# Optimization experiments

Measured on AMD Instinct MI355X. Metric: run time of the kernel, lower is better.

Reference implementation:

```python
import jax, jax.numpy as jnp
import numpy as np
from jax import lax

B, N = 8, 8192
H, W = 512, 512
C = 192          # backbone feature channels (Swin-L stage 1)
HF, WF = 128, 128  # H/4, W/4
STATE = 256
VLR = 3
STRIDE = 4.0
DOWN = 4.0
EPS = 1e-8


def bilinear_sample(feat, poly, h, w):
    """F.grid_sample(align_corners=True, bilinear) equivalent.
    feat: (B,C,h,w), poly: (B,N,2) pixel coords -> (B,C,N)."""
    gx = poly[..., 0] / (w / 2.0) - 1.0
    gy = poly[..., 1] / (h / 2.0) - 1.0
    x = (gx + 1.0) * 0.5 * (w - 1)   # align_corners=True unnormalize
    y = (gy + 1.0) * 0.5 * (h - 1)
    x0 = jnp.floor(x); y0 = jnp.floor(y)
    fx = x - x0; fy = y - y0
    x0i = jnp.clip(x0, 0, w - 1).astype(jnp.int32)
    x1i = jnp.clip(x0 + 1, 0, w - 1).astype(jnp.int32)
    y0i = jnp.clip(y0, 0, h - 1).astype(jnp.int32)
    y1i = jnp.clip(y0 + 1, 0, h - 1).astype(jnp.int32)
    b = jnp.arange(feat.shape[0])[:, None]
    f00 = feat[b, :, y0i, x0i]  # (B,N,C)
    f01 = feat[b, :, y0i, x1i]
    f10 = feat[b, :, y1i, x0i]
    f11 = feat[b, :, y1i, x1i]
    w00 = ((1 - fy) * (1 - fx))[..., None]
    w01 = ((1 - fy) * fx)[..., None]
    w10 = (fy * (1 - fx))[..., None]
    w11 = (fy * fx)[..., None]
    out = f00 * w00 + f01 * w01 + f10 * w10 + f11 * w11  # (B,N,C)
    return jnp.transpose(out, (0, 2, 1))  # (B,C,N)


def mlp3(x, W1, b1, W2, b2, W3, b3):
    """per-point MLP (1x1 conv stack). x: (B,Cin,N) -> (B,Cout,N)."""
    h1 = jax.nn.relu(jnp.einsum('oc,bcn->bon', W1, x) + b1[None, :, None])
    h2 = jax.nn.relu(jnp.einsum('oc,bcn->bon', W2, h1) + b2[None, :, None])
    return jnp.einsum('oc,bcn->bon', W3, h2) + b3[None, :, None]


def can_poly(poly, mask):
    # canonical poly: subtract per-polygon masked min of valid points
    big = jnp.float32(1e9)
    masked = jnp.where(mask[..., None] > 0, poly, big)
    mins = jnp.min(masked, axis=1, keepdims=True)  # (B,1,2)
    return (poly - mins) * mask[..., None]


def polygon_angles(poly, mask):
    prev = jnp.roll(poly, 1, axis=1)
    nxt = jnp.roll(poly, -1, axis=1)
    v1 = prev - poly
    v2 = nxt - poly
    dot = jnp.sum(v1 * v2, axis=-1)
    nrm = jnp.linalg.norm(v1, axis=-1) * jnp.linalg.norm(v2, axis=-1)
    cosang = jnp.clip(dot / (nrm + EPS), -1.0, 1.0)
    return jnp.arccos(cosang) * mask  # (B,N)


def setup_inputs() -> dict:
    key = jax.random.key(0)
    ks = jax.random.split(key, 20)
    DIN_OFF = C + 2   # 194
    DIN_CLS = C + 3   # 195
    inp = {
        'image': jax.random.normal(ks[0], (B, 3, H, W), jnp.float32),
        'pred_points': jax.random.uniform(ks[1], (B, N, 2), jnp.float32) * (WF - 1),
        'valid_mask': jnp.ones((B, N), jnp.float32),
        'bw': jax.random.normal(ks[2], (C, 3, 4, 4), jnp.float32) * 0.05,
        'bb': jnp.zeros((C,), jnp.float32),
        'off_W1': jax.random.normal(ks[3], (VLR, STATE, DIN_OFF), jnp.float32) * 0.02,
        'off_b1': jnp.zeros((VLR, STATE), jnp.float32),
        'off_W2': jax.random.normal(ks[4], (VLR, STATE, STATE), jnp.float32) * 0.02,
        'off_b2': jnp.zeros((VLR, STATE), jnp.float32),
        'off_W3': jax.random.normal(ks[5], (VLR, 2, STATE), jnp.float32) * 0.02,
        'off_b3': jnp.zeros((VLR, 2), jnp.float32),
        'cls_W1': jax.random.normal(ks[6], (STATE, DIN_CLS), jnp.float32) * 0.02,
        'cls_b1': jnp.zeros((STATE,), jnp.float32),
        'cls_W2': jax.random.normal(ks[7], (STATE, STATE), jnp.float32) * 0.02,
        'cls_b2': jnp.zeros((STATE,), jnp.float32),
        'cls_W3': jax.random.normal(ks[8], (1, STATE), jnp.float32) * 0.02,
        'cls_b3': jnp.zeros((1,), jnp.float32),
    }
    return inp


def reference(image, pred_points, valid_mask, bw, bb,
              off_W1, off_b1, off_W2, off_b2, off_W3, off_b3,
              cls_W1, cls_b1, cls_W2, cls_b2, cls_W3, cls_b3):
    # frozen backbone stand-in (torch.no_grad on swin_l): stride-4 patch-embed conv
    feat = lax.conv_general_dilated(
        image, bw, window_strides=(4, 4), padding='VALID',
        dimension_numbers=('NCHW', 'OIHW', 'NCHW')) + bb[None, :, None, None]
    feat = lax.stop_gradient(feat)  # (B,C,HF,WF)

    py = pred_points
    for i in range(VLR):
        c_py = can_poly(py, valid_mask)
        g = bilinear_sample(feat, py, HF, WF) * valid_mask[:, None, :]   # (B,C,N)
        x = jnp.concatenate([g, jnp.transpose(c_py, (0, 2, 1))], axis=1)  # (B,C+2,N)
        off = mlp3(x, off_W1[i], off_b1[i], off_W2[i], off_b2[i], off_W3[i], off_b3[i])
        off = jnp.transpose(off, (0, 2, 1)) * valid_mask[..., None]      # (B,N,2)
        py = py + off * STRIDE

    gf = bilinear_sample(feat, py, HF, WF) * valid_mask[:, None, :]      # (B,C,N)
    angles = lax.stop_gradient(polygon_angles(py, valid_mask))           # (B,N)
    cls_feat = jnp.concatenate(
        [gf, jnp.transpose(py, (0, 2, 1)), angles[:, None, :]], axis=1)  # (B,C+3,N)
    logits = mlp3(cls_feat, cls_W1, cls_b1, cls_W2, cls_b2, cls_W3, cls_b3)  # (B,1,N)
    cls_points = logits[:, 0, :] * valid_mask                            # (B,N)

    final_refined_points = py * DOWN
    return (final_refined_points, cls_points)
```

## Files before the change

kernel.cpp:

```cpp
#include <hip/hip_runtime.h>
#include <hip/hip_bf16.h>
#include <hip/hip_fp8.h>

#define NB 8
#define NP 8192
#define IMH 512
#define IMW 512
#define NC 192
#define FH 128
#define FW 128
#define NSTATE 256

#define P1 232
#define P2 264
#define K1PAD 224
#define CPITCH 72

typedef __attribute__((ext_vector_type(8))) unsigned short ush8;
typedef __attribute__((ext_vector_type(8))) short short8v;
typedef __attribute__((ext_vector_type(4))) float f32x4;

__device__ __forceinline__ float bf2f(unsigned short u) {
  return __uint_as_float(((unsigned)u) << 16);
}
__device__ __forceinline__ float fp8tof(unsigned char b) {
  __hip_fp8_e4m3 v;
  v.__x = b;
  return (float)v;
}
__device__ __forceinline__ unsigned char ftofp8(float f) {
  __hip_fp8_e4m3 v(f);
  return v.__x;
}
__device__ __forceinline__ unsigned fenc(float f) {
  unsigned u = __float_as_uint(f);
  return (u & 0x80000000u) ? ~u : (u | 0x80000000u);
}
__device__ __forceinline__ float fdec(unsigned u) {
  return __uint_as_float((u & 0x80000000u) ? (u & 0x7FFFFFFFu) : ~u);
}

__global__ __launch_bounds__(256) void conv_kernel(
    const float* __restrict__ img, const __hip_bfloat16* __restrict__ wcb,
    const float* __restrict__ bb, unsigned char* __restrict__ feat) {
  __shared__ __hip_bfloat16 Xim[64 * CPITCH];

  const int tid = threadIdx.x;
  const int lane = tid & 63;
  const int w = tid >> 6;
  const int cl = lane & 15;
  const int kg = lane >> 4;
  const int b = blockIdx.x & 7;
  const int pix0 = (blockIdx.x >> 3) * 64;
  const int y = pix0 >> 7;
  const int xh = (pix0 >> 6) & 1;

  {
    const int pix = tid & 63;
    const int q = tid >> 6;
    *(uint2*)&Xim[pix * CPITCH + 48 + q * 4] = (uint2){0u, 0u};
  }

#pragma unroll
  for (int it = 0; it < 3; ++it) {
    const int idx = it * 256 + tid;
    const int row = idx >> 6;
    const int c = idx & 63;
    const int ci = row >> 2, ky = row & 3;
    const float4 v = *(const float4*)(img + (((size_t)b * 3 + ci) * IMH +
                                             (y * 4 + ky)) * IMW + xh * 256 + c * 4);
    __hip_bfloat16 h[4];
    h[0] = __float2bfloat16(v.x);
    h[1] = __float2bfloat16(v.y);
    h[2] = __float2bfloat16(v.z);
    h[3] = __float2bfloat16(v.w);
    *(uint2*)&Xim[c * CPITCH + ci * 16 + ky * 4] = *(const uint2*)h;
  }
  __syncthreads();

  f32x4 acc[4][3];
#pragma unroll
  for (int mt = 0; mt < 4; ++mt)
#pragma unroll
    for (int nt = 0; nt < 3; ++nt) acc[mt][nt] = (f32x4){0, 0, 0, 0};

#pragma unroll
  for (int kc = 0; kc < 2; ++kc) {
    short8v af[4], bfv[3];
#pragma unroll
    for (int mt = 0; mt < 4; ++mt)
      af[mt] = *(const short8v*)&Xim[(mt * 16 + cl) * CPITCH + kc * 32 + kg * 8];
#pragma unroll
    for (int nt = 0; nt < 3; ++nt)
      bfv[nt] = *(const short8v*)&wcb[(size_t)(w * 48 + nt * 16 + cl) * 64 +
                                      kc * 32 + kg * 8];
#pragma unroll
    for (int mt = 0; mt < 4; ++mt)
#pragma unroll
      for (int nt = 0; nt < 3; ++nt)
        acc[mt][nt] = __builtin_amdgcn_mfma_f32_16x16x32_bf16(
            af[mt], bfv[nt], acc[mt][nt], 0, 0, 0);
  }

#pragma unroll
  for (int nt = 0; nt < 3; ++nt) {
    const float bias = bb[w * 48 + nt * 16 + cl];
#pragma unroll
    for (int mt = 0; mt < 4; ++mt) {
#pragma unroll
      for (int r = 0; r < 4; ++r) {
        feat[((size_t)(w * 8 + b) * 16384 + pix0 + mt * 16 + kg * 4 + r) * 48 +
             nt * 16 + cl] = ftofp8(acc[mt][nt][r] + bias);
      }
    }
  }
}

__global__ void prep_all_kernel(
    const float* __restrict__ oW1, const float* __restrict__ cW1,
    const float* __restrict__ oW2, const float* __restrict__ cW2,
    const float* __restrict__ bw, const float* __restrict__ pred,
    const float* __restrict__ mask, __hip_bfloat16* __restrict__ w1b,
    __hip_bfloat16* __restrict__ w2b, __hip_bfloat16* __restrict__ wcb,
    unsigned* __restrict__ mins4) {
  __shared__ float sx[4], sy[4];
  const int idx = blockIdx.x * 256 + threadIdx.x;
  const int region = blockIdx.y;
  if (region == 0) {
    if (idx >= 4 * 256 * P1) return;
    const int L = idx / (256 * P1);
    const int rem = idx - L * (256 * P1);
    const int n = rem / P1;
    const int k = rem - n * P1;
    const float* src = (L < 3) ? (oW1 + (size_t)L * 256 * 194) : cW1;
    const int K = (L < 3) ? 194 : 195;
    w1b[idx] = __float2bfloat16((k < K) ? src[(size_t)n * K + k] : 0.0f);
  } else if (region == 1) {
    if (idx >= 4 * 256 * P2) return;
    const int L = idx / (256 * P2);
    const int rem = idx - L * (256 * P2);
    const int n = rem / P2;
    const int k = rem - n * P2;
    const float* src = (L < 3) ? (oW2 + (size_t)L * 65536) : cW2;
    w2b[idx] = __float2bfloat16((k < 256) ? src[(size_t)n * 256 + k] : 0.0f);
  } else if (region == 2) {
    if (idx < 48) mins4[16 + idx] = fenc(1e9f);
    if (idx >= 192 * 64) return;
    const int n = idx >> 6;
    const int k = idx & 63;
    wcb[idx] = __float2bfloat16((k < 48) ? bw[(size_t)n * 48 + k] : 0.0f);
  } else {
    if (blockIdx.x >= 8) return;
    const int b = blockIdx.x;
    float mx = 1e9f, my = 1e9f;
    for (int n = threadIdx.x; n < NP; n += 256) {
      float m = mask[(size_t)b * NP + n];
      float2 p = *(const float2*)&pred[((size_t)b * NP + n) * 2];
      mx = fminf(mx, m > 0.0f ? p.x : 1e9f);
      my = fminf(my, m > 0.0f ? p.y : 1e9f);
    }
#pragma unroll
    for (int o = 32; o > 0; o >>= 1) {
      mx = fminf(mx, __shfl_down(mx, o));
      my = fminf(my, __shfl_down(my, o));
    }
    if ((threadIdx.x & 63) == 0) {
      sx[threadIdx.x >> 6] = mx;
      sy[threadIdx.x >> 6] = my;
    }
    __syncthreads();
    if (threadIdx.x == 0) {
      mx = fminf(fminf(sx[0], sx[1]), fminf(sx[2], sx[3]));
      my = fminf(fminf(sy[0], sy[1]), fminf(sy[2], sy[3]));
      mins4[b * 2 + 0] = fenc(mx);
      mins4[b * 2 + 1] = fenc(my);
    }
  }
}

template <bool CLS>
__global__ __launch_bounds__(256, 2) void mlp_kernel(
    const unsigned char* __restrict__ feat,
    const float* __restrict__ p_in,
    const float* __restrict__ mask,
    const unsigned* __restrict__ mins_in,
    unsigned* __restrict__ mins_out,
    const __hip_bfloat16* __restrict__ W1b, const float* __restrict__ b1,
    const __hip_bfloat16* __restrict__ W2b, const float* __restrict__ b2,
    const float* __restrict__ W3, const float* __restrict__ b3,
    float* __restrict__ out0) {
  __shared__ __hip_bfloat16 Xls[64 * P2];
  __shared__ float red[4][64][2];

  const int tid = threadIdx.x;
  const int lane = tid & 63;
  const int w = tid >> 6;
  const int cl = lane & 15;
  const int kg = lane >> 4;
  const int b = blockIdx.x & 7;
  const int m0 = (blockIdx.x >> 3) * 64;

  {
    const int m = tid >> 2;
    const int j = tid & 3;
    const int n = m0 + m;
    const size_t pidx = (size_t)b * NP + n;
    const float msk = mask[pidx];
    const float2 pv = *(const float2*)&p_in[pidx * 2];
    const float px = pv.x, pyv = pv.y;
    const float xs = px * (127.0f / 128.0f);
    const float ys = pyv * (127.0f / 128.0f);
    const float x0f = floorf(xs), y0f = floorf(ys);
    const float fx = xs - x0f, fy = ys - y0f;
    const int x0 = (int)fminf(fmaxf(x0f, 0.0f), 127.0f);
    const int x1 = (int)fminf(fmaxf(x0f + 1.0f, 0.0f), 127.0f);
    const int y0 = (int)fminf(fmaxf(y0f, 0.0f), 127.0f);
    const int y1 = (int)fminf(fmaxf(y0f + 1.0f, 0.0f), 127.0f);
    const float w00 = (1.0f - fy) * (1.0f - fx);
    const float w01 = (1.0f - fy) * fx;
    const float w10 = fy * (1.0f - fx);
    const float w11 = fy * fx;
    const unsigned char* fb = feat + (size_t)(j * 8 + b) * 16384 * 48;
    const uint4* r00 = (const uint4*)(fb + (size_t)(y0 * FW + x0) * 48);
    const uint4* r01 = (const uint4*)(fb + (size_t)(y0 * FW + x1) * 48);
    const uint4* r10 = (const uint4*)(fb + (size_t)(y1 * FW + x0) * 48);
    const uint4* r11 = (const uint4*)(fb + (size_t)(y1 * FW + x1) * 48);
#pragma unroll
    for (int v = 0; v < 3; ++v) {
      union { uint4 u; unsigned char c[16]; } a0, a1, a2, a3;
      a0.u = r00[v]; a1.u = r01[v]; a2.u = r10[v]; a3.u = r11[v];
      __hip_bfloat16 h[16];
#pragma unroll
      for (int e = 0; e < 16; ++e) {
        float gg = w00 * fp8tof(a0.c[e]) + w01 * fp8tof(a1.c[e]) +
                   w10 * fp8tof(a2.c[e]) + w11 * fp8tof(a3.c[e]);
        h[e] = __float2bfloat16(gg * msk);
      }
      *(ush8*)&Xls[m * P1 + j * 48 + v * 16 + 0] = *(const ush8*)&h[0];
      *(ush8*)&Xls[m * P1 + j * 48 + v * 16 + 8] = *(const ush8*)&h[8];
    }
    if (j == 0) {
      __hip_bfloat16 ex[32];
#pragma unroll
      for (int i = 0; i < 32; ++i) ex[i] = __float2bfloat16(0.0f);
      if constexpr (!CLS) {
        ex[0] = __float2bfloat16((px - fdec(mins_in[b * 2 + 0])) * msk);
        ex[1] = __float2bfloat16((pyv - fdec(mins_in[b * 2 + 1])) * msk);
      } else {
        ex[0] = __float2bfloat16(px);
        ex[1] = __float2bfloat16(pyv);
        const int npv = (n + NP - 1) & (NP - 1);
        const int nnx = (n + 1) & (NP - 1);
        const float2 pp = *(const float2*)&p_in[((size_t)b * NP + npv) * 2];
        const float2 pn = *(const float2*)&p_in[((size_t)b * NP + nnx) * 2];
        const float v1x = pp.x - px, v1y = pp.y - pyv;
        const float v2x = pn.x - px, v2y = pn.y - pyv;
        const float dot = v1x * v2x + v1y * v2y;
        const float nrm =
            sqrtf(v1x * v1x + v1y * v1y) * sqrtf(v2x * v2x + v2y * v2y);
        const float ca = fminf(fmaxf(dot / (nrm + 1e-8f), -1.0f), 1.0f);
        ex[2] = __float2bfloat16(acosf(ca) * msk);
      }
#pragma unroll
      for (int q = 0; q < 4; ++q)
        *(ush8*)&Xls[m * P1 + 192 + q * 8] = *(const ush8*)&ex[q * 8];
    }
  }

  short8v w1f[7][4];
#pragma unroll
  for (int kc = 0; kc < 7; ++kc)
#pragma unroll
    for (int nt = 0; nt < 4; ++nt)
      w1f[kc][nt] = *(const short8v*)&W1b[(size_t)(w * 64 + nt * 16 + cl) * P1 +
                                          kc * 32 + kg * 8];
  float b1v[4], b2v[4], w3av[4], w3bv[4];
#pragma unroll
  for (int nt = 0; nt < 4; ++nt) {
    const int n = w * 64 + nt * 16 + cl;
    b1v[nt] = b1[n];
    b2v[nt] = b2[n];
    w3av[nt] = W3[n];
    w3bv[nt] = CLS ? 0.0f : W3[256 + n];
  }
  __syncthreads();

  f32x4 acc[4][4];
#pragma unroll
  for (int mt = 0; mt < 4; ++mt)
#pragma unroll
    for (int nt = 0; nt < 4; ++nt) acc[mt][nt] = (f32x4){0, 0, 0, 0};

#pragma unroll
  for (int kc = 0; kc < 7; ++kc) {
    short8v af[4];
#pragma unroll
    for (int mt = 0; mt < 4; ++mt)
      af[mt] = *(const short8v*)&Xls[(mt * 16 + cl) * P1 + kc * 32 + kg * 8];
#pragma unroll
    for (int mt = 0; mt < 4; ++mt)
#pragma unroll
      for (int nt = 0; nt < 4; ++nt)
        acc[mt][nt] = __builtin_amdgcn_mfma_f32_16x16x32_bf16(
            af[mt], w1f[kc][nt], acc[mt][nt], 0, 0, 0);
  }

  short8v w2f[8][4];
#pragma unroll
  for (int kc = 0; kc < 8; ++kc)
#pragma unroll
    for (int nt = 0; nt < 4; ++nt)
      w2f[kc][nt] = *(const short8v*)&W2b[(size_t)(w * 64 + nt * 16 + cl) * P2 +
                                          kc * 32 + kg * 8];
  __syncthreads();

#pragma unroll
  for (int nt = 0; nt < 4; ++nt) {
    const float bias = b1v[nt];
    const int n = w * 64 + nt * 16 + cl;
#pragma unroll
    for (int mt = 0; mt < 4; ++mt) {
#pragma unroll
      for (int r = 0; r < 4; ++r) {
        const float v = fmaxf(acc[mt][nt][r] + bias, 0.0f);
        Xls[(mt * 16 + kg * 4 + r) * P2 + n] = __float2bfloat16(v);
      }
    }
  }
  __syncthreads();

  f32x4 acc2[4][4];
#pragma unroll
  for (int mt = 0; mt < 4; ++mt)
#pragma unroll
    for (int nt = 0; nt < 4; ++nt) acc2[mt][nt] = (f32x4){0, 0, 0, 0};

#pragma unroll
  for (int kc = 0; kc < 8; ++kc) {
    short8v af[4];
#pragma unroll
    for (int mt = 0; mt < 4; ++mt)
      af[mt] = *(const short8v*)&Xls[(mt * 16 + cl) * P2 + kc * 32 + kg * 8];
#pragma unroll
    for (int mt = 0; mt < 4; ++mt)
#pragma unroll
      for (int nt = 0; nt < 4; ++nt)
        acc2[mt][nt] = __builtin_amdgcn_mfma_f32_16x16x32_bf16(
            af[mt], w2f[kc][nt], acc2[mt][nt], 0, 0, 0);
  }

  float pr[4][4][2];
#pragma unroll
  for (int mt = 0; mt < 4; ++mt)
#pragma unroll
    for (int r = 0; r < 4; ++r) { pr[mt][r][0] = 0.0f; pr[mt][r][1] = 0.0f; }

#pragma unroll
  for (int nt = 0; nt < 4; ++nt) {
    const float bias = b2v[nt];
    const float w3a = w3av[nt];
    const float w3b = w3bv[nt];
#pragma unroll
    for (int mt = 0; mt < 4; ++mt) {
#pragma unroll
      for (int r = 0; r < 4; ++r) {
        const float t = fmaxf(acc2[mt][nt][r] + bias, 0.0f);
        pr[mt][r][0] = fmaf(t, w3a, pr[mt][r][0]);
        if constexpr (!CLS) pr[mt][r][1] = fmaf(t, w3b, pr[mt][r][1]);
      }
    }
  }
#pragma unroll
  for (int s = 1; s < 16; s <<= 1) {
#pragma unroll
    for (int mt = 0; mt < 4; ++mt)
#pragma unroll
      for (int r = 0; r < 4; ++r) {
        pr[mt][r][0] += __shfl_xor(pr[mt][r][0], s);
        if constexpr (!CLS) pr[mt][r][1] += __shfl_xor(pr[mt][r][1], s);
      }
  }
  if constexpr (!CLS) {
    if (cl < 8) {
      const int r = cl >> 1, o = cl & 1;
#pragma unroll
      for (int mt = 0; mt < 4; ++mt)
        red[w][mt * 16 + kg * 4 + r][o] = pr[mt][r][o];
    }
  } else {
    if (cl < 4) {
      const int r = cl;
#pragma unroll
      for (int mt = 0; mt < 4; ++mt)
        red[w][mt * 16 + kg * 4 + r][0] = pr[mt][r][0];
    }
  }
  __syncthreads();

  if constexpr (!CLS) {
    if (tid < 128) {
      const int m = tid >> 1, o = tid & 1;
      const float s = red[0][m][o] + red[1][m][o] + red[2][m][o] + red[3][m][o];
      const size_t pidx = (size_t)b * NP + m0 + m;
      const float msk = mask[pidx];
      const float off = (s + b3[o]) * msk;
      const float nv = p_in[pidx * 2 + o] + off * 4.0f;
      out0[pidx * 2 + o] = nv;
      float mval = (msk > 0.0f) ? nv : 1e9f;
#pragma unroll
      for (int st = 2; st < 64; st <<= 1)
        mval = fminf(mval, __shfl_xor(mval, st));
      if ((tid & 63) < 2 && mins_out != nullptr)
        atomicMin(&mins_out[b * 2 + o], fenc(mval));
    }
  } else {
    if (tid < 64) {
      const int m = tid;
      const float s = red[0][m][0] + red[1][m][0] + red[2][m][0] + red[3][m][0];
      const size_t pidx = (size_t)b * NP + m0 + m;
      const float msk = mask[pidx];
      out0[pidx * 2 + 0] = p_in[pidx * 2 + 0] * 4.0f;
      out0[pidx * 2 + 1] = p_in[pidx * 2 + 1] * 4.0f;
      out0[(size_t)2 * NB * NP + pidx] = (s + b3[0]) * msk;
    }
  }
}

extern "C" void kernel_launch(void* const* d_in, const int* in_sizes, int n_in,
                              void* d_out, int out_size, void* d_ws,
                              size_t ws_size, hipStream_t stream) {
  const float* image = (const float*)d_in[0];
  const float* pred  = (const float*)d_in[1];
  const float* mask  = (const float*)d_in[2];
  const float* bw    = (const float*)d_in[3];
  const float* bb    = (const float*)d_in[4];
  const float* oW1   = (const float*)d_in[5];
  const float* ob1   = (const float*)d_in[6];
  const float* oW2   = (const float*)d_in[7];
  const float* ob2   = (const float*)d_in[8];
  const float* oW3   = (const float*)d_in[9];
  const float* ob3   = (const float*)d_in[10];
  const float* cW1   = (const float*)d_in[11];
  const float* cb1   = (const float*)d_in[12];
  const float* cW2   = (const float*)d_in[13];
  const float* cb2   = (const float*)d_in[14];
  const float* cW3   = (const float*)d_in[15];
  const float* cb3   = (const float*)d_in[16];
  float* out = (float*)d_out;

  char* ws = (char*)d_ws;
  unsigned char* feat = (unsigned char*)ws;
  const size_t featB = (size_t)NB * FH * FW * NC;
  float* pyA  = (float*)(ws + featB);
  float* pyB  = pyA + (size_t)NB * NP * 2;
  unsigned* mins4 = (unsigned*)(pyB + (size_t)NB * NP * 2);
  __hip_bfloat16* w1b = (__hip_bfloat16*)(mins4 + 64);
  __hip_bfloat16* w2b = w1b + (size_t)4 * 256 * P1;
  __hip_bfloat16* wcb = w2b + (size_t)4 * 256 * P2;

  prep_all_kernel<<<dim3(1056, 4), 256, 0, stream>>>(
      oW1, cW1, oW2, cW2, bw, pred, mask, w1b, w2b, wcb, mins4);
  conv_kernel<<<dim3(NB * 16384 / 64), 256, 0, stream>>>(image, wcb, bb, feat);

  const float* cur = pred;
  float* nxt = pyA;
  for (int i = 0; i < 3; ++i) {
    mlp_kernel<false><<<dim3(NB * NP / 64), 256, 0, stream>>>(
        feat, cur, mask, mins4 + i * 16,
        (i < 2) ? (mins4 + (i + 1) * 16) : nullptr,
        w1b + (size_t)i * 256 * P1, ob1 + (size_t)i * NSTATE,
        w2b + (size_t)i * 256 * P2, ob2 + (size_t)i * NSTATE,
        oW3 + (size_t)i * 2 * NSTATE, ob3 + (size_t)i * 2, nxt);
    cur = nxt;
    nxt = (nxt == pyA) ? pyB : pyA;
  }
  mlp_kernel<true><<<dim3(NB * NP / 64), 256, 0, stream>>>(
      feat, cur, mask, nullptr, nullptr, w1b + (size_t)3 * 256 * P1, cb1,
      w2b + (size_t)3 * 256 * P2, cb2, cW3, cb3, out);
}
```

Before: 208.2 us.

## Double MLP block to 512 threads, split output columns across eight waves

```diff
diff --git a/kernel.cpp b/kernel.cpp
--- a/kernel.cpp
+++ b/kernel.cpp
@@ -179,7 +179,7 @@
 }
 
 template <bool CLS>
-__global__ __launch_bounds__(256, 2) void mlp_kernel(
+__global__ __launch_bounds__(512, 2) void mlp_kernel(
     const unsigned char* __restrict__ feat,
     const float* __restrict__ p_in,
     const float* __restrict__ mask,
@@ -190,7 +190,7 @@
     const float* __restrict__ W3, const float* __restrict__ b3,
     float* __restrict__ out0) {
   __shared__ __hip_bfloat16 Xls[64 * P2];
-  __shared__ float red[4][64][2];
+  __shared__ float red[8][64][2];
 
   const int tid = threadIdx.x;
   const int lane = tid & 63;
@@ -199,10 +199,13 @@
   const int kg = lane >> 4;
   const int b = blockIdx.x & 7;
   const int m0 = (blockIdx.x >> 3) * 64;
+  const int nbase = w * 32;
 
   {
-    const int m = tid >> 2;
-    const int j = tid & 3;
+    const int m = tid >> 3;
+    const int s = tid & 7;
+    const int j4 = s >> 1;
+    const int h = s & 1;
     const int n = m0 + m;
     const size_t pidx = (size_t)b * NP + n;
     const float msk = mask[pidx];
@@ -220,26 +223,35 @@
     const float w01 = (1.0f - fy) * fx;
     const float w10 = fy * (1.0f - fx);
     const float w11 = fy * fx;
-    const unsigned char* fb = feat + (size_t)(j * 8 + b) * 16384 * 48;
-    const uint4* r00 = (const uint4*)(fb + (size_t)(y0 * FW + x0) * 48);
-    const uint4* r01 = (const uint4*)(fb + (size_t)(y0 * FW + x1) * 48);
-    const uint4* r10 = (const uint4*)(fb + (size_t)(y1 * FW + x0) * 48);
-    const uint4* r11 = (const uint4*)(fb + (size_t)(y1 * FW + x1) * 48);
+    const unsigned char* fb =
+        feat + (size_t)(j4 * 8 + b) * 16384 * 48 + h * 24;
+    const unsigned char* r00 = fb + (size_t)(y0 * FW + x0) * 48;
+    const unsigned char* r01 = fb + (size_t)(y0 * FW + x1) * 48;
+    const unsigned char* r10 = fb + (size_t)(y1 * FW + x0) * 48;
+    const unsigned char* r11 = fb + (size_t)(y1 * FW + x1) * 48;
 #pragma unroll
     for (int v = 0; v < 3; ++v) {
-      union { uint4 u; unsigned char c[16]; } a0, a1, a2, a3;
-      a0.u = r00[v]; a1.u = r01[v]; a2.u = r10[v]; a3.u = r11[v];
-      __hip_bfloat16 h[16];
-#pragma unroll
-      for (int e = 0; e < 16; ++e) {
-        float gg = w00 * fp8tof(a0.c[e]) + w01 * fp8tof(a1.c[e]) +
-                   w10 * fp8tof(a2.c[e]) + w11 * fp8tof(a3.c[e]);
-        h[e] = __float2bfloat16(gg * msk);
-      }
-      *(ush8*)&Xls[m * P1 + j * 48 + v * 16 + 0] = *(const ush8*)&h[0];
-      *(ush8*)&Xls[m * P1 + j * 48 + v * 16 + 8] = *(const ush8*)&h[8];
-    }
-    if (j == 0) {
+      const uint2 a0 = *(const uint2*)(r00 + v * 8);
+      const uint2 a1 = *(const uint2*)(r01 + v * 8);
+      const uint2 a2 = *(const uint2*)(r10 + v * 8);
+      const uint2 a3 = *(const uint2*)(r11 + v * 8);
+      __hip_bfloat16 hh[8];
+#pragma unroll
+      for (int e = 0; e < 8; ++e) {
+        const int sh = (e & 3) * 8;
+        const unsigned d0 = (e < 4) ? a0.x : a0.y;
+        const unsigned d1 = (e < 4) ? a1.x : a1.y;
+        const unsigned d2 = (e < 4) ? a2.x : a2.y;
+        const unsigned d3 = (e < 4) ? a3.x : a3.y;
+        float gg = w00 * fp8tof((d0 >> sh) & 0xff) +
+                   w01 * fp8tof((d1 >> sh) & 0xff) +
+                   w10 * fp8tof((d2 >> sh) & 0xff) +
+                   w11 * fp8tof((d3 >> sh) & 0xff);
+        hh[e] = __float2bfloat16(gg * msk);
+      }
+      *(ush8*)&Xls[m * P1 + j4 * 48 + h * 24 + v * 8] = *(const ush8*)hh;
+    }
+    if (s == 0) {
       __hip_bfloat16 ex[32];
 #pragma unroll
       for (int i = 0; i < 32; ++i) ex[i] = __float2bfloat16(0.0f);
@@ -267,17 +279,17 @@
     }
   }
 
-  short8v w1f[7][4];
+  short8v w1f[7][2];
 #pragma unroll
   for (int kc = 0; kc < 7; ++kc)
 #pragma unroll
-    for (int nt = 0; nt < 4; ++nt)
-      w1f[kc][nt] = *(const short8v*)&W1b[(size_t)(w * 64 + nt * 16 + cl) * P1 +
+    for (int nt = 0; nt < 2; ++nt)
+      w1f[kc][nt] = *(const short8v*)&W1b[(size_t)(nbase + nt * 16 + cl) * P1 +
                                           kc * 32 + kg * 8];
-  float b1v[4], b2v[4], w3av[4], w3bv[4];
-#pragma unroll
-  for (int nt = 0; nt < 4; ++nt) {
-    const int n = w * 64 + nt * 16 + cl;
+  float b1v[2], b2v[2], w3av[2], w3bv[2];
+#pragma unroll
+  for (int nt = 0; nt < 2; ++nt) {
+    const int n = nbase + nt * 16 + cl;
     b1v[nt] = b1[n];
     b2v[nt] = b2[n];
     w3av[nt] = W3[n];
@@ -285,11 +297,11 @@
   }
   __syncthreads();
 
-  f32x4 acc[4][4];
+  f32x4 acc[4][2];
 #pragma unroll
   for (int mt = 0; mt < 4; ++mt)
 #pragma unroll
-    for (int nt = 0; nt < 4; ++nt) acc[mt][nt] = (f32x4){0, 0, 0, 0};
+    for (int nt = 0; nt < 2; ++nt) acc[mt][nt] = (f32x4){0, 0, 0, 0};
 
 #pragma unroll
   for (int kc = 0; kc < 7; ++kc) {
@@ -300,24 +312,24 @@
 #pragma unroll
     for (int mt = 0; mt < 4; ++mt)
 #pragma unroll
-      for (int nt = 0; nt < 4; ++nt)
+      for (int nt = 0; nt < 2; ++nt)
         acc[mt][nt] = __builtin_amdgcn_mfma_f32_16x16x32_bf16(
             af[mt], w1f[kc][nt], acc[mt][nt], 0, 0, 0);
   }
 
-  short8v w2f[8][4];
+  short8v w2f[8][2];
 #pragma unroll
   for (int kc = 0; kc < 8; ++kc)
 #pragma unroll
-    for (int nt = 0; nt < 4; ++nt)
-      w2f[kc][nt] = *(const short8v*)&W2b[(size_t)(w * 64 + nt * 16 + cl) * P2 +
+    for (int nt = 0; nt < 2; ++nt)
+      w2f[kc][nt] = *(const short8v*)&W2b[(size_t)(nbase + nt * 16 + cl) * P2 +
                                           kc * 32 + kg * 8];
   __syncthreads();
 
 #pragma unroll
-  for (int nt = 0; nt < 4; ++nt) {
+  for (int nt = 0; nt < 2; ++nt) {
     const float bias = b1v[nt];
-    const int n = w * 64 + nt * 16 + cl;
+    const int n = nbase + nt * 16 + cl;
 #pragma unroll
     for (int mt = 0; mt < 4; ++mt) {
 #pragma unroll
@@ -329,11 +341,11 @@
   }
   __syncthreads();
 
-  f32x4 acc2[4][4];
+  f32x4 acc2[4][2];
 #pragma unroll
   for (int mt = 0; mt < 4; ++mt)
 #pragma unroll
-    for (int nt = 0; nt < 4; ++nt) acc2[mt][nt] = (f32x4){0, 0, 0, 0};
+    for (int nt = 0; nt < 2; ++nt) acc2[mt][nt] = (f32x4){0, 0, 0, 0};
 
 #pragma unroll
   for (int kc = 0; kc < 8; ++kc) {
@@ -344,7 +356,7 @@
 #pragma unroll
     for (int mt = 0; mt < 4; ++mt)
 #pragma unroll
-      for (int nt = 0; nt < 4; ++nt)
+      for (int nt = 0; nt < 2; ++nt)
         acc2[mt][nt] = __builtin_amdgcn_mfma_f32_16x16x32_bf16(
             af[mt], w2f[kc][nt], acc2[mt][nt], 0, 0, 0);
   }
@@ -356,7 +368,7 @@
     for (int r = 0; r < 4; ++r) { pr[mt][r][0] = 0.0f; pr[mt][r][1] = 0.0f; }
 
 #pragma unroll
-  for (int nt = 0; nt < 4; ++nt) {
+  for (int nt = 0; nt < 2; ++nt) {
     const float bias = b2v[nt];
     const float w3a = w3av[nt];
     const float w3b = w3bv[nt];
@@ -400,7 +412,9 @@
   if constexpr (!CLS) {
     if (tid < 128) {
       const int m = tid >> 1, o = tid & 1;
-      const float s = red[0][m][o] + red[1][m][o] + red[2][m][o] + red[3][m][o];
+      float s = 0.0f;
+#pragma unroll
+      for (int ww = 0; ww < 8; ++ww) s += red[ww][m][o];
       const size_t pidx = (size_t)b * NP + m0 + m;
       const float msk = mask[pidx];
       const float off = (s + b3[o]) * msk;
@@ -416,7 +430,9 @@
   } else {
     if (tid < 64) {
       const int m = tid;
-      const float s = red[0][m][0] + red[1][m][0] + red[2][m][0] + red[3][m][0];
+      float s = 0.0f;
+#pragma unroll
+      for (int ww = 0; ww < 8; ++ww) s += red[ww][m][0];
       const size_t pidx = (size_t)b * NP + m0 + m;
       const float msk = mask[pidx];
       out0[pidx * 2 + 0] = p_in[pidx * 2 + 0] * 4.0f;
@@ -465,7 +481,7 @@
   const float* cur = pred;
   float* nxt = pyA;
   for (int i = 0; i < 3; ++i) {
-    mlp_kernel<false><<<dim3(NB * NP / 64), 256, 0, stream>>>(
+    mlp_kernel<false><<<dim3(NB * NP / 64), 512, 0, stream>>>(
         feat, cur, mask, mins4 + i * 16,
         (i < 2) ? (mins4 + (i + 1) * 16) : nullptr,
         w1b + (size_t)i * 256 * P1, ob1 + (size_t)i * NSTATE,
@@ -474,7 +490,7 @@
     cur = nxt;
     nxt = (nxt == pyA) ? pyB : pyA;
   }
-  mlp_kernel<true><<<dim3(NB * NP / 64), 256, 0, stream>>>(
+  mlp_kernel<true><<<dim3(NB * NP / 64), 512, 0, stream>>>(
       feat, cur, mask, nullptr, nullptr, w1b + (size_t)3 * 256 * P1, cb1,
       w2b + (size_t)3 * 256 * P2, cb2, cW3, cb3, out);
 }
```

Result: slower. 217.1 us (+4.2%).

## Pre-swizzle MLP weights into MFMA fragment order and stream per k-chunk

Applied to the files above, without the earlier changes.

```diff
diff --git a/kernel.cpp b/kernel.cpp
--- a/kernel.cpp
+++ b/kernel.cpp
@@ -15,6 +15,8 @@
 #define P2 264
 #define K1PAD 224
 #define CPITCH 72
+#define W1FRAG 57344
+#define W2FRAG 65536
 
 typedef __attribute__((ext_vector_type(8))) unsigned short ush8;
 typedef __attribute__((ext_vector_type(8))) short short8v;
@@ -120,29 +122,41 @@
     const float* __restrict__ oW1, const float* __restrict__ cW1,
     const float* __restrict__ oW2, const float* __restrict__ cW2,
     const float* __restrict__ bw, const float* __restrict__ pred,
-    const float* __restrict__ mask, __hip_bfloat16* __restrict__ w1b,
-    __hip_bfloat16* __restrict__ w2b, __hip_bfloat16* __restrict__ wcb,
+    const float* __restrict__ mask, __hip_bfloat16* __restrict__ w1c,
+    __hip_bfloat16* __restrict__ w2c, __hip_bfloat16* __restrict__ wcb,
     unsigned* __restrict__ mins4) {
   __shared__ float sx[4], sy[4];
   const int idx = blockIdx.x * 256 + threadIdx.x;
   const int region = blockIdx.y;
   if (region == 0) {
-    if (idx >= 4 * 256 * P1) return;
-    const int L = idx / (256 * P1);
-    const int rem = idx - L * (256 * P1);
-    const int n = rem / P1;
-    const int k = rem - n * P1;
+    if (idx >= 4 * W1FRAG) return;
+    const int L = idx / W1FRAG;
+    const int rem = idx - L * W1FRAG;
+    const int kc = rem >> 13;
+    const int r2 = rem & 8191;
+    const int ng = r2 >> 9;
+    const int r3 = r2 & 511;
+    const int lane = r3 >> 3;
+    const int e = r3 & 7;
+    const int n = ng * 16 + (lane & 15);
+    const int k = kc * 32 + (lane >> 4) * 8 + e;
     const float* src = (L < 3) ? (oW1 + (size_t)L * 256 * 194) : cW1;
     const int K = (L < 3) ? 194 : 195;
-    w1b[idx] = __float2bfloat16((k < K) ? src[(size_t)n * K + k] : 0.0f);
+    w1c[idx] = __float2bfloat16((k < K) ? src[(size_t)n * K + k] : 0.0f);
   } else if (region == 1) {
-    if (idx >= 4 * 256 * P2) return;
-    const int L = idx / (256 * P2);
-    const int rem = idx - L * (256 * P2);
-    const int n = rem / P2;
-    const int k = rem - n * P2;
+    if (idx >= 4 * W2FRAG) return;
+    const int L = idx >> 16;
+    const int rem = idx & 65535;
+    const int kc = rem >> 13;
+    const int r2 = rem & 8191;
+    const int ng = r2 >> 9;
+    const int r3 = r2 & 511;
+    const int lane = r3 >> 3;
+    const int e = r3 & 7;
+    const int n = ng * 16 + (lane & 15);
+    const int k = kc * 32 + (lane >> 4) * 8 + e;
     const float* src = (L < 3) ? (oW2 + (size_t)L * 65536) : cW2;
-    w2b[idx] = __float2bfloat16((k < 256) ? src[(size_t)n * 256 + k] : 0.0f);
+    w2c[idx] = __float2bfloat16(src[(size_t)n * 256 + k]);
   } else if (region == 2) {
     if (idx < 48) mins4[16 + idx] = fenc(1e9f);
     if (idx >= 192 * 64) return;
@@ -179,14 +193,14 @@
 }
 
 template <bool CLS>
-__global__ __launch_bounds__(256, 2) void mlp_kernel(
+__global__ __launch_bounds__(256, 4) void mlp_kernel(
     const unsigned char* __restrict__ feat,
     const float* __restrict__ p_in,
     const float* __restrict__ mask,
     const unsigned* __restrict__ mins_in,
     unsigned* __restrict__ mins_out,
-    const __hip_bfloat16* __restrict__ W1b, const float* __restrict__ b1,
-    const __hip_bfloat16* __restrict__ W2b, const float* __restrict__ b2,
+    const __hip_bfloat16* __restrict__ W1c, const float* __restrict__ b1,
+    const __hip_bfloat16* __restrict__ W2c, const float* __restrict__ b2,
     const float* __restrict__ W3, const float* __restrict__ b3,
     float* __restrict__ out0) {
   __shared__ __hip_bfloat16 Xls[64 * P2];
@@ -267,13 +281,6 @@
     }
   }
 
-  short8v w1f[7][4];
-#pragma unroll
-  for (int kc = 0; kc < 7; ++kc)
-#pragma unroll
-    for (int nt = 0; nt < 4; ++nt)
-      w1f[kc][nt] = *(const short8v*)&W1b[(size_t)(w * 64 + nt * 16 + cl) * P1 +
-                                          kc * 32 + kg * 8];
   float b1v[4], b2v[4], w3av[4], w3bv[4];
 #pragma unroll
   for (int nt = 0; nt < 4; ++nt) {
@@ -293,7 +300,10 @@
 
 #pragma unroll
   for (int kc = 0; kc < 7; ++kc) {
-    short8v af[4];
+    short8v af[4], bfv[4];
+#pragma unroll
+    for (int nt = 0; nt < 4; ++nt)
+      bfv[nt] = *(const short8v*)&W1c[kc * 8192 + (w * 4 + nt) * 512 + lane * 8];
 #pragma unroll
     for (int mt = 0; mt < 4; ++mt)
       af[mt] = *(const short8v*)&Xls[(mt * 16 + cl) * P1 + kc * 32 + kg * 8];
@@ -302,16 +312,8 @@
 #pragma unroll
       for (int nt = 0; nt < 4; ++nt)
         acc[mt][nt] = __builtin_amdgcn_mfma_f32_16x16x32_bf16(
-            af[mt], w1f[kc][nt], acc[mt][nt], 0, 0, 0);
-  }
-
-  short8v w2f[8][4];
-#pragma unroll
-  for (int kc = 0; kc < 8; ++kc)
-#pragma unroll
-    for (int nt = 0; nt < 4; ++nt)
-      w2f[kc][nt] = *(const short8v*)&W2b[(size_t)(w * 64 + nt * 16 + cl) * P2 +
-                                          kc * 32 + kg * 8];
+            af[mt], bfv[nt], acc[mt][nt], 0, 0, 0);
+  }
   __syncthreads();
 
 #pragma unroll
@@ -337,7 +339,10 @@
 
 #pragma unroll
   for (int kc = 0; kc < 8; ++kc) {
-    short8v af[4];
+    short8v af[4], bfv[4];
+#pragma unroll
+    for (int nt = 0; nt < 4; ++nt)
+      bfv[nt] = *(const short8v*)&W2c[kc * 8192 + (w * 4 + nt) * 512 + lane * 8];
 #pragma unroll
     for (int mt = 0; mt < 4; ++mt)
       af[mt] = *(const short8v*)&Xls[(mt * 16 + cl) * P2 + kc * 32 + kg * 8];
@@ -346,7 +351,7 @@
 #pragma unroll
       for (int nt = 0; nt < 4; ++nt)
         acc2[mt][nt] = __builtin_amdgcn_mfma_f32_16x16x32_bf16(
-            af[mt], w2f[kc][nt], acc2[mt][nt], 0, 0, 0);
+            af[mt], bfv[nt], acc2[mt][nt], 0, 0, 0);
   }
 
   float pr[4][4][2];
@@ -454,12 +459,12 @@
   float* pyA  = (float*)(ws + featB);
   float* pyB  = pyA + (size_t)NB * NP * 2;
   unsigned* mins4 = (unsigned*)(pyB + (size_t)NB * NP * 2);
-  __hip_bfloat16* w1b = (__hip_bfloat16*)(mins4 + 64);
-  __hip_bfloat16* w2b = w1b + (size_t)4 * 256 * P1;
-  __hip_bfloat16* wcb = w2b + (size_t)4 * 256 * P2;
-
-  prep_all_kernel<<<dim3(1056, 4), 256, 0, stream>>>(
-      oW1, cW1, oW2, cW2, bw, pred, mask, w1b, w2b, wcb, mins4);
+  __hip_bfloat16* w1c = (__hip_bfloat16*)(mins4 + 64);
+  __hip_bfloat16* w2c = w1c + (size_t)4 * W1FRAG;
+  __hip_bfloat16* wcb = w2c + (size_t)4 * W2FRAG;
+
+  prep_all_kernel<<<dim3(1024, 4), 256, 0, stream>>>(
+      oW1, cW1, oW2, cW2, bw, pred, mask, w1c, w2c, wcb, mins4);
   conv_kernel<<<dim3(NB * 16384 / 64), 256, 0, stream>>>(image, wcb, bb, feat);
 
   const float* cur = pred;
@@ -468,13 +473,13 @@
     mlp_kernel<false><<<dim3(NB * NP / 64), 256, 0, stream>>>(
         feat, cur, mask, mins4 + i * 16,
         (i < 2) ? (mins4 + (i + 1) * 16) : nullptr,
-        w1b + (size_t)i * 256 * P1, ob1 + (size_t)i * NSTATE,
-        w2b + (size_t)i * 256 * P2, ob2 + (size_t)i * NSTATE,
+        w1c + (size_t)i * W1FRAG, ob1 + (size_t)i * NSTATE,
+        w2c + (size_t)i * W2FRAG, ob2 + (size_t)i * NSTATE,
         oW3 + (size_t)i * 2 * NSTATE, ob3 + (size_t)i * 2, nxt);
     cur = nxt;
     nxt = (nxt == pyA) ? pyB : pyA;
   }
   mlp_kernel<true><<<dim3(NB * NP / 64), 256, 0, stream>>>(
-      feat, cur, mask, nullptr, nullptr, w1b + (size_t)3 * 256 * P1, cb1,
-      w2b + (size_t)3 * 256 * P2, cb2, cW3, cb3, out);
-}
+      feat, cur, mask, nullptr, nullptr, w1c + (size_t)3 * W1FRAG, cb1,
+      w2c + (size_t)3 * W2FRAG, cb2, cW3, cb3, out);
+}
```

After: 221.5 us. 6.4% more time.
